# Kernel tuning notes

Hardware: AMD Instinct MI355X
Metric: run time of the kernel (lower is better)

## Reference

```python
import jax, jax.numpy as jnp
import numpy as np

B, S, E = 2, 2048, 1024
H = 16
HD = E // H           # 64
KD = 64               # k_dim
VD = 64               # v_dim
SCALE = 1.0 / np.float32(np.sqrt(KD))


def setup_inputs() -> dict:
    key = jax.random.key(0)
    ks = jax.random.split(key, 10)
    return {
        "x": jax.random.normal(ks[0], (B, S, E), dtype=jnp.float32),
        "mask": jax.random.uniform(ks[1], (S, S), dtype=jnp.float32),
        "Wq": jax.random.normal(ks[2], (HD, KD), dtype=jnp.float32) * 0.05,
        "bq": jax.random.normal(ks[3], (KD,), dtype=jnp.float32) * 0.05,
        "Wk": jax.random.normal(ks[4], (HD, KD), dtype=jnp.float32) * 0.05,
        "bk": jax.random.normal(ks[5], (KD,), dtype=jnp.float32) * 0.05,
        "Wv": jax.random.normal(ks[6], (HD, VD), dtype=jnp.float32) * 0.05,
        "bv": jax.random.normal(ks[7], (VD,), dtype=jnp.float32) * 0.05,
        "Wo": jax.random.normal(ks[8], (H * VD, E), dtype=jnp.float32) * 0.05,
        "bo": jax.random.normal(ks[9], (E,), dtype=jnp.float32) * 0.05,
    }


def reference(x, mask, Wq, bq, Wk, bk, Wv, bv, Wo, bo):
    b, s, e = x.shape
    # (B, S, E) -> (B, H, S, head_dim)
    xh = x.reshape(b, s, H, HD).transpose(0, 2, 1, 3)
    q = jnp.einsum('bhsd,dk->bhsk', xh, Wq) + bq   # (B,H,S,KD)
    k = jnp.einsum('bhsd,dk->bhsk', xh, Wk) + bk   # (B,H,S,KD)
    v = jnp.einsum('bhsd,dv->bhsv', xh, Wv) + bv   # (B,H,S,VD)
    sim = jnp.einsum('bhqk,bhsk->bhqs', q, k) * SCALE  # (B,H,S,S)
    sim = sim * mask[None, None, :, :]                  # multiplicative mask
    attn = jax.nn.softmax(sim, axis=-1)
    out = jnp.einsum('bhqs,bhsv->bhqv', attn, v)        # (B,H,S,VD)
    out = out.transpose(0, 2, 1, 3).reshape(b, s, H * VD)
    return out @ Wo + bo
```

## Files before the change

kernel.cpp:

```cpp
#include <hip/hip_runtime.h>
#include <hip/hip_bf16.h>

#define SS 2048
#define EE 1024
#define SCALE 0.125f
#define LOG2E 1.44269504088896f

typedef __attribute__((ext_vector_type(8))) short short8;
typedef __attribute__((ext_vector_type(4))) float float4v;
typedef __attribute__((ext_vector_type(4))) unsigned int uint4v;

__device__ __forceinline__ unsigned short f2bf(float f) {
  unsigned int u = __float_as_uint(f);
  unsigned int lsb = (u >> 16) & 1u;
  u += 0x7fffu + lsb;
  return (unsigned short)(u >> 16);
}
__device__ __forceinline__ unsigned int pk2bf(float a, float b) {
  __hip_bfloat162 h = __float22bfloat162_rn(float2{a, b});
  return *reinterpret_cast<unsigned int*>(&h);
}

__global__ __launch_bounds__(256) void prep_kernel(
    const float* __restrict__ mask,
    const float* __restrict__ Wq, const float* __restrict__ Wk,
    const float* __restrict__ Wv,
    unsigned short* __restrict__ maskP, unsigned short* __restrict__ W3T)
{
  __shared__ unsigned short t[64 * 65];
  int blk = blockIdx.x;
  int tid = threadIdx.x;
  if (blk < 2048) {
    int idx = blk * 256 + tid;
    int lane = idx & 63, step = (idx >> 6) & 63, qt = idx >> 12;
    int li = lane & 15, g = lane >> 4;
    const float c = SCALE * LOG2E;
    const float* mrow = mask + (size_t)(qt * 16 + li) * SS + step * 32 + g * 4;
    float4 a = *(const float4*)mrow;
    float4 bb = *(const float4*)(mrow + 16);
    uint4v o;
    o.x = pk2bf(a.x * c, a.y * c);
    o.y = pk2bf(a.z * c, a.w * c);
    o.z = pk2bf(bb.x * c, bb.y * c);
    o.w = pk2bf(bb.z * c, bb.w * c);
    *(uint4v*)(maskP + (size_t)idx * 8) = o;
    return;
  }
  int m = blk - 2048;
  const float* W = (m == 0) ? Wq : (m == 1 ? Wk : Wv);
#pragma unroll
  for (int i = 0; i < 16; ++i) {
    int e = tid + i * 256; int d = e >> 6, n = e & 63;
    t[n * 65 + d] = f2bf(W[e]);
  }
  __syncthreads();
  unsigned short* dst = W3T + m * 4096;
#pragma unroll
  for (int i = 0; i < 16; ++i) {
    int e = tid + i * 256; int n = e >> 6, d = e & 63;
    dst[n * 64 + d] = t[n * 65 + d];
  }
}

__global__ __launch_bounds__(256) void qkv_kernel(
    const float* __restrict__ x, const unsigned short* __restrict__ W3T,
    const float* __restrict__ bq, const float* __restrict__ bk,
    const float* __restrict__ bv,
    unsigned short* __restrict__ Q, unsigned short* __restrict__ Kp,
    unsigned short* __restrict__ Vf)
{
  __shared__ __align__(16) unsigned short w3t[192 * 72];
  __shared__ __align__(16) unsigned short xt[64 * 72];
  __shared__ __align__(16) unsigned short ob[12288];
  __shared__ float sBias[192];
  int tid = threadIdx.x;
  int bh = blockIdx.x >> 4;
  int s0blk = (blockIdx.x & 15) * 128;
  int b = bh >> 4, h = bh & 15;
  int wv = tid >> 6, lane = tid & 63;
  int li = lane & 15, g = lane >> 4;

#pragma unroll
  for (int i = 0; i < 6; ++i) {
    int slot = tid + i * 256;
    int row = slot >> 3, c = slot & 7;
    *(short8*)(w3t + row * 72 + c * 8) = *(const short8*)(W3T + slot * 8);
  }
  if (tid < 192) sBias[tid] = (tid < 64) ? bq[tid] : (tid < 128 ? bk[tid - 64] : bv[tid - 128]);

  for (int half = 0; half < 2; ++half) {
    int s0 = s0blk + half * 64;
    if (half) __syncthreads();
    const float* xbase = x + ((size_t)(b * SS + s0)) * EE + h * 64;
#pragma unroll
    for (int it = 0; it < 4; ++it) {
      int flat = tid + it * 256;
      int row = flat >> 4, ch = flat & 15;
      float4 v = *(const float4*)(xbase + (size_t)row * EE + ch * 4);
      uint2 u; u.x = pk2bf(v.x, v.y); u.y = pk2bf(v.z, v.w);
      *(uint2*)(xt + row * 72 + ch * 4) = u;
    }
    __syncthreads();

    int mrow = wv * 16;
    short8 af[2];
#pragma unroll
    for (int ks = 0; ks < 2; ++ks)
      af[ks] = *(const short8*)(xt + (mrow + li) * 72 + ks * 32 + g * 8);

    float4v acc[12];
#pragma unroll
    for (int i = 0; i < 12; ++i) acc[i] = (float4v){0, 0, 0, 0};
#pragma unroll
    for (int ks = 0; ks < 2; ++ks)
#pragma unroll
      for (int nb = 0; nb < 12; ++nb) {
        short8 bfr = *(const short8*)(w3t + (nb * 16 + li) * 72 + ks * 32 + g * 8);
        acc[nb] = __builtin_amdgcn_mfma_f32_16x16x32_bf16(af[ks], bfr, acc[nb], 0, 0, 0);
      }

#pragma unroll
    for (int nb = 0; nb < 12; ++nb) {
      float bias = sBias[nb * 16 + li];
      int mtx = nb >> 2, sub = nb & 3;
#pragma unroll
      for (int r = 0; r < 4; ++r) {
        unsigned short v = f2bf(acc[nb][r] + bias);
        int sl = mrow + g * 4 + r;
        int stp = sl >> 5, s5 = sl & 31;
        if (mtx == 0) {
          ob[sl * 64 + sub * 16 + li] = v;
        } else if (mtx == 1) {
          int sb = s5 >> 4, lik = s5 & 15;
          int part = sub >> 1;
          int gk = ((sub & 1) << 1) | (li >> 3);
          ob[4096 + stp * 2048 + (sb * 2 + part) * 512 + (gk * 16 + lik) * 8 + (li & 7)] = v;
        } else {
          int pos = ((s5 >> 2) & 3) * 8 + ((s5 >> 4) & 1) * 4 + (s5 & 3);
          ob[8192 + stp * 2048 + sub * 512 + ((pos >> 3) * 16 + li) * 8 + (pos & 7)] = v;
        }
      }
    }
    __syncthreads();

    unsigned short* Qg = Q + ((size_t)bh * SS + s0) * 64;
    unsigned short* Kg = Kp + (size_t)bh * 131072 + (s0 >> 5) * 2048;
    unsigned short* Vg = Vf + (size_t)bh * 131072 + (s0 >> 5) * 2048;
#pragma unroll
    for (int i = 0; i < 6; ++i) {
      int slot = tid + i * 256;
      int rgn = slot >> 9, off = (slot & 511) * 8;
      short8 v = *(const short8*)(ob + rgn * 4096 + off);
      unsigned short* dst = (rgn == 0) ? (Qg + off) : (rgn == 1 ? (Kg + off) : (Vg + off));
      *(short8*)dst = v;
    }
  }
}

__global__ __launch_bounds__(256) void attn_kernel(
    const unsigned short* __restrict__ Q, const unsigned short* __restrict__ Kp,
    const unsigned short* __restrict__ Vf, const unsigned short* __restrict__ maskP,
    unsigned short* __restrict__ AO)
{
  __shared__ __align__(16) unsigned short tr_all[4 * 32 * 72];
  int tid = threadIdx.x, wv = tid >> 6, lane = tid & 63;
  int li = lane & 15, g = lane >> 4;
  int wave_id = blockIdx.x * 4 + wv;
  int bh = wave_id >> 6;
  int q0 = (wave_id & 63) * 32;

  short8 qf[2][2];
#pragma unroll
  for (int t = 0; t < 2; ++t) {
    const unsigned short* Qb = Q + ((size_t)bh * SS + q0 + t * 16 + li) * 64;
    qf[t][0] = *(const short8*)(Qb + g * 8);
    qf[t][1] = *(const short8*)(Qb + 32 + g * 8);
  }

  const unsigned short* Kg = Kp + (size_t)bh * 131072 + lane * 8;
  const unsigned short* Vg = Vf + (size_t)bh * 131072 + lane * 8;
  const unsigned short* Mg0 = maskP + (size_t)(q0 >> 4) * 32768 + lane * 8;
  const unsigned short* Mg1 = Mg0 + 32768;

  unsigned short ov = (li == 0) ? (unsigned short)0x3F80 : (unsigned short)0;
  short8 vones = {(short)ov, (short)ov, (short)ov, (short)ov,
                  (short)ov, (short)ov, (short)ov, (short)ov};

  float4v acc[2][4];
#pragma unroll
  for (int t = 0; t < 2; ++t)
#pragma unroll
    for (int nb = 0; nb < 4; ++nb) acc[t][nb] = (float4v){0, 0, 0, 0};
  float4v accd[2] = {{0, 0, 0, 0}, {0, 0, 0, 0}};

  float4v st[2][2];

  short8 kA[4], kB[4], vA[4], vB[4];
  uint4v mA0, mA1, mB0, mB1;
  {
    short8 k0[4];
#pragma unroll
    for (int i = 0; i < 4; ++i) {
      k0[i] = *(const short8*)(Kg + i * 512);
      kA[i] = *(const short8*)(Kg + 2048 + i * 512);
      kB[i] = *(const short8*)(Kg + 2 * 2048 + i * 512);
      vA[i] = *(const short8*)(Vg + i * 512);
      vB[i] = *(const short8*)(Vg + 2048 + i * 512);
    }
    mA0 = *(const uint4v*)Mg0;
    mA1 = *(const uint4v*)Mg1;
    mB0 = *(const uint4v*)(Mg0 + 512);
    mB1 = *(const uint4v*)(Mg1 + 512);
#pragma unroll
    for (int t = 0; t < 2; ++t)
#pragma unroll
      for (int sb = 0; sb < 2; ++sb) {
        float4v s = {0, 0, 0, 0};
        s = __builtin_amdgcn_mfma_f32_16x16x32_bf16(k0[sb * 2], qf[t][0], s, 0, 0, 0);
        s = __builtin_amdgcn_mfma_f32_16x16x32_bf16(k0[sb * 2 + 1], qf[t][1], s, 0, 0, 0);
        st[t][sb] = s;
      }
  }

  auto half_step = [&](short8 (&kf)[4], short8 (&vf)[4], uint4v& m0c, uint4v& m1c,
                       int kn, int vn, int mn) {
    short8 pf[2];
#pragma unroll
    for (int t = 0; t < 2; ++t) {
      uint4v pw2;
#pragma unroll
      for (int sb = 0; sb < 2; ++sb) {
#pragma unroll
        for (int hh = 0; hh < 2; ++hh) {
          unsigned int mm = (t == 0) ? m0c[sb * 2 + hh] : m1c[sb * 2 + hh];
          float p0 = __builtin_amdgcn_exp2f(st[t][sb][2 * hh] * __uint_as_float(mm << 16));
          float p1 = __builtin_amdgcn_exp2f(st[t][sb][2 * hh + 1] * __uint_as_float(mm & 0xffff0000u));
          pw2[sb * 2 + hh] = pk2bf(p0, p1);
        }
      }
      pf[t] = *(short8*)&pw2;
    }
    m0c = *(const uint4v*)(Mg0 + (size_t)mn * 512);
    m1c = *(const uint4v*)(Mg1 + (size_t)mn * 512);
#pragma unroll
    for (int t = 0; t < 2; ++t)
#pragma unroll
      for (int sb = 0; sb < 2; ++sb) {
        float4v s = {0, 0, 0, 0};
        s = __builtin_amdgcn_mfma_f32_16x16x32_bf16(kf[sb * 2], qf[t][0], s, 0, 0, 0);
        s = __builtin_amdgcn_mfma_f32_16x16x32_bf16(kf[sb * 2 + 1], qf[t][1], s, 0, 0, 0);
        st[t][sb] = s;
      }
#pragma unroll
    for (int i = 0; i < 4; ++i)
      kf[i] = *(const short8*)(Kg + (size_t)kn * 2048 + i * 512);
#pragma unroll
    for (int nb = 0; nb < 4; ++nb) {
      acc[0][nb] = __builtin_amdgcn_mfma_f32_16x16x32_bf16(vf[nb], pf[0], acc[0][nb], 0, 0, 0);
      acc[1][nb] = __builtin_amdgcn_mfma_f32_16x16x32_bf16(vf[nb], pf[1], acc[1][nb], 0, 0, 0);
    }
    accd[0] = __builtin_amdgcn_mfma_f32_16x16x32_bf16(vones, pf[0], accd[0], 0, 0, 0);
    accd[1] = __builtin_amdgcn_mfma_f32_16x16x32_bf16(vones, pf[1], accd[1], 0, 0, 0);
#pragma unroll
    for (int i = 0; i < 4; ++i)
      vf[i] = *(const short8*)(Vg + (size_t)vn * 2048 + i * 512);
  };

  for (int su = 0; su < 32; ++su) {
    half_step(kA, vA, mA0, mA1, (2 * su + 3) & 63, (2 * su + 2) & 63, (2 * su + 2) & 63);
    half_step(kB, vB, mB0, mB1, (2 * su + 4) & 63, (2 * su + 3) & 63, (2 * su + 3) & 63);
  }

  unsigned short* tr = tr_all + wv * (32 * 72);
#pragma unroll
  for (int t = 0; t < 2; ++t) {
    float den = __shfl(accd[t][0], li, 64);
    float rd = 1.0f / den;
#pragma unroll
    for (int nb = 0; nb < 4; ++nb) {
      int base = (t * 16 + li) * 72 + nb * 16 + g * 4;
      *(unsigned int*)(tr + base)     = pk2bf(acc[t][nb][0] * rd, acc[t][nb][1] * rd);
      *(unsigned int*)(tr + base + 2) = pk2bf(acc[t][nb][2] * rd, acc[t][nb][3] * rd);
    }
  }
  asm volatile("s_waitcnt lgkmcnt(0)" ::: "memory");

  int b = bh >> 4, h = bh & 15;
  int rrow = lane >> 3, part = lane & 7;
#pragma unroll
  for (int i = 0; i < 4; ++i) {
    int row = i * 8 + rrow;
    short8 o = *(const short8*)(tr + row * 72 + part * 8);
    *(short8*)(AO + ((size_t)(b * SS + q0 + row)) * EE + h * 64 + part * 8) = o;
  }
}

__global__ __launch_bounds__(256) void out_gemm(
    const unsigned short* __restrict__ AO, const float* __restrict__ Wo,
    const float* __restrict__ bo, float* __restrict__ out)
{
  __shared__ __align__(16) unsigned short at[128 * 72];
  __shared__ __align__(16) unsigned short bt[64 * 72];
  int tid = threadIdx.x, wv = tid >> 6, lane = tid & 63;
  int li = lane & 15, g = lane >> 4;
  int m0 = (blockIdx.x >> 4) * 128;
  int n0 = (blockIdx.x & 15) * 64;
  int wm = (wv & 1) * 64, wn = (wv >> 1) * 32;

  const unsigned short* Ag = AO + (size_t)m0 * 1024;
  const float* Bg = Wo + n0;
  int srow = tid >> 3, scol = (tid & 7) * 8;
  int bkrow = tid >> 4, bch = tid & 15;

  short8 apre[4];
  float4 bpre[4];
  auto ldst = [&](int k0) {
#pragma unroll
    for (int i = 0; i < 4; ++i)
      apre[i] = *(const short8*)(Ag + (size_t)(srow + i * 32) * 1024 + k0 + scol);
#pragma unroll
    for (int i = 0; i < 4; ++i)
      bpre[i] = *(const float4*)(Bg + (size_t)(k0 + bkrow + i * 16) * 1024 + bch * 4);
  };

  float4v acc[4][2];
#pragma unroll
  for (int mt = 0; mt < 4; ++mt)
#pragma unroll
    for (int nt = 0; nt < 2; ++nt) acc[mt][nt] = (float4v){0, 0, 0, 0};

  ldst(0);
  for (int k0 = 0; k0 < 1024; k0 += 64) {
    __syncthreads();
#pragma unroll
    for (int i = 0; i < 4; ++i)
      *(short8*)(at + (srow + i * 32) * 72 + scol) = apre[i];
#pragma unroll
    for (int i = 0; i < 4; ++i) {
      int kr = bkrow + i * 16;
      float4 v = bpre[i];
      bt[(bch * 4 + 0) * 72 + kr] = f2bf(v.x);
      bt[(bch * 4 + 1) * 72 + kr] = f2bf(v.y);
      bt[(bch * 4 + 2) * 72 + kr] = f2bf(v.z);
      bt[(bch * 4 + 3) * 72 + kr] = f2bf(v.w);
    }
    int nk = (k0 + 64 < 1024) ? k0 + 64 : 0;
    ldst(nk);
    __syncthreads();
#pragma unroll
    for (int ks = 0; ks < 2; ++ks) {
      short8 afr[4], bfr[2];
#pragma unroll
      for (int mt = 0; mt < 4; ++mt)
        afr[mt] = *(const short8*)(at + (wm + mt * 16 + li) * 72 + ks * 32 + g * 8);
#pragma unroll
      for (int nt = 0; nt < 2; ++nt)
        bfr[nt] = *(const short8*)(bt + (wn + nt * 16 + li) * 72 + ks * 32 + g * 8);
#pragma unroll
      for (int mt = 0; mt < 4; ++mt)
#pragma unroll
        for (int nt = 0; nt < 2; ++nt)
          acc[mt][nt] = __builtin_amdgcn_mfma_f32_16x16x32_bf16(afr[mt], bfr[nt], acc[mt][nt], 0, 0, 0);
    }
  }
#pragma unroll
  for (int nt = 0; nt < 2; ++nt) {
    float bof = bo[n0 + wn + nt * 16 + li];
#pragma unroll
    for (int mt = 0; mt < 4; ++mt)
#pragma unroll
      for (int r = 0; r < 4; ++r)
        out[(size_t)(m0 + wm + mt * 16 + g * 4 + r) * 1024 + n0 + wn + nt * 16 + li] =
            acc[mt][nt][r] + bof;
  }
}

extern "C" void kernel_launch(void* const* d_in, const int* in_sizes, int n_in,
                              void* d_out, int out_size, void* d_ws, size_t ws_size,
                              hipStream_t stream) {
  const float* x    = (const float*)d_in[0];
  const float* mask = (const float*)d_in[1];
  const float* Wq   = (const float*)d_in[2];
  const float* bq   = (const float*)d_in[3];
  const float* Wk   = (const float*)d_in[4];
  const float* bk   = (const float*)d_in[5];
  const float* Wv   = (const float*)d_in[6];
  const float* bv   = (const float*)d_in[7];
  const float* Wo   = (const float*)d_in[8];
  const float* bo   = (const float*)d_in[9];
  float* out = (float*)d_out;

  unsigned short* ws = (unsigned short*)d_ws;
  unsigned short* Q     = ws;
  unsigned short* Kp    = ws + 4194304;
  unsigned short* Vf    = ws + 8388608;
  unsigned short* AO    = ws + 12582912;
  unsigned short* maskP = ws + 16777216;
  unsigned short* W3T = AO;

  prep_kernel<<<2051, 256, 0, stream>>>(mask, Wq, Wk, Wv, maskP, W3T);
  qkv_kernel<<<512, 256, 0, stream>>>(x, W3T, bq, bk, bv, Q, Kp, Vf);
  attn_kernel<<<512, 256, 0, stream>>>(Q, Kp, Vf, maskP, AO);
  out_gemm<<<512, 256, 0, stream>>>(AO, Wo, bo, out);
}
```

Before: 191.5 us.

## Stage K/V tiles in shared memory cooperatively and remap blocks for L2 locality

Instead of each wave loading its own K and V tiles straight from global memory into registers, the four waves of a block now cooperatively load one K/V tile pair into a double-buffered LDS region and all read from it. This cuts redundant global traffic by four, since all waves in a block share the same head. Blocks are also remapped so consecutively scheduled blocks spread across heads, to change L2/XCD locality. The cost is a __syncthreads per step and LDS read latency in the inner loop, plus the register-level prefetch depth is reduced.

```diff
diff --git a/kernel.cpp b/kernel.cpp
--- a/kernel.cpp
+++ b/kernel.cpp
@@ -162,10 +162,11 @@
     const unsigned short* __restrict__ Vf, const unsigned short* __restrict__ maskP,
     unsigned short* __restrict__ AO)
 {
-  __shared__ __align__(16) unsigned short tr_all[4 * 32 * 72];
+  __shared__ __align__(16) unsigned short smem[9216];
   int tid = threadIdx.x, wv = tid >> 6, lane = tid & 63;
   int li = lane & 15, g = lane >> 4;
-  int wave_id = blockIdx.x * 4 + wv;
+  int virt = (blockIdx.x & 7) * 64 + (blockIdx.x >> 3);
+  int wave_id = virt * 4 + wv;
   int bh = wave_id >> 6;
   int q0 = (wave_id & 63) * 32;
 
@@ -177,8 +178,12 @@
     qf[t][1] = *(const short8*)(Qb + 32 + g * 8);
   }
 
-  const unsigned short* Kg = Kp + (size_t)bh * 131072 + lane * 8;
-  const unsigned short* Vg = Vf + (size_t)bh * 131072 + lane * 8;
+  const unsigned short* stgsrc =
+      ((wv < 2) ? (Kp + (size_t)bh * 131072) : (Vf + (size_t)bh * 131072)) +
+      (wv & 1) * 1024 + lane * 8;
+  unsigned short* srd = smem + lane * 8;
+  unsigned short* swr = smem + wv * 1024 + lane * 8;
+
   const unsigned short* Mg0 = maskP + (size_t)(q0 >> 4) * 32768 + lane * 8;
   const unsigned short* Mg1 = Mg0 + 32768;
 
@@ -194,23 +199,26 @@
   float4v accd[2] = {{0, 0, 0, 0}, {0, 0, 0, 0}};
 
   float4v st[2][2];
-
-  short8 kA[4], kB[4], vA[4], vB[4];
-  uint4v mA0, mA1, mB0, mB1;
+  short8 vf[4];
+  uint4v mc0, mc1;
+
+  mc0 = *(const uint4v*)Mg0;
+  mc1 = *(const uint4v*)Mg1;
+  {
+    short8 a0 = *(const short8*)(stgsrc);
+    short8 a1 = *(const short8*)(stgsrc + 512);
+    short8 b0 = *(const short8*)(stgsrc + 2048);
+    short8 b1 = *(const short8*)(stgsrc + 2048 + 512);
+    *(short8*)(swr + 0) = a0;
+    *(short8*)(swr + 512) = a1;
+    *(short8*)(swr + 4096) = b0;
+    *(short8*)(swr + 4096 + 512) = b1;
+  }
+  __syncthreads();
   {
     short8 k0[4];
 #pragma unroll
-    for (int i = 0; i < 4; ++i) {
-      k0[i] = *(const short8*)(Kg + i * 512);
-      kA[i] = *(const short8*)(Kg + 2048 + i * 512);
-      kB[i] = *(const short8*)(Kg + 2 * 2048 + i * 512);
-      vA[i] = *(const short8*)(Vg + i * 512);
-      vB[i] = *(const short8*)(Vg + 2048 + i * 512);
-    }
-    mA0 = *(const uint4v*)Mg0;
-    mA1 = *(const uint4v*)Mg1;
-    mB0 = *(const uint4v*)(Mg0 + 512);
-    mB1 = *(const uint4v*)(Mg1 + 512);
+    for (int i = 0; i < 4; ++i) k0[i] = *(const short8*)(srd + i * 512);
 #pragma unroll
     for (int t = 0; t < 2; ++t)
 #pragma unroll
@@ -220,40 +228,39 @@
         s = __builtin_amdgcn_mfma_f32_16x16x32_bf16(k0[sb * 2 + 1], qf[t][1], s, 0, 0, 0);
         st[t][sb] = s;
       }
-  }
-
-  auto half_step = [&](short8 (&kf)[4], short8 (&vf)[4], uint4v& m0c, uint4v& m1c,
-                       int kn, int vn, int mn) {
+#pragma unroll
+    for (int i = 0; i < 4; ++i) vf[i] = *(const short8*)(srd + 2048 + i * 512);
+  }
+  __syncthreads();
+
+  auto body = [&](int s, int pcur, bool do_stage) {
+    short8 sg0, sg1;
+    if (do_stage) {
+      const unsigned short* gs = stgsrc + (size_t)(s + 2) * 2048;
+      sg0 = *(const short8*)gs;
+      sg1 = *(const short8*)(gs + 512);
+    }
+    short8 kf[4];
+#pragma unroll
+    for (int i = 0; i < 4; ++i)
+      kf[i] = *(const short8*)(srd + pcur * 4096 + i * 512);
     short8 pf[2];
 #pragma unroll
     for (int t = 0; t < 2; ++t) {
       uint4v pw2;
 #pragma unroll
-      for (int sb = 0; sb < 2; ++sb) {
+      for (int sb = 0; sb < 2; ++sb)
 #pragma unroll
         for (int hh = 0; hh < 2; ++hh) {
-          unsigned int mm = (t == 0) ? m0c[sb * 2 + hh] : m1c[sb * 2 + hh];
+          unsigned int mm = (t == 0) ? mc0[sb * 2 + hh] : mc1[sb * 2 + hh];
           float p0 = __builtin_amdgcn_exp2f(st[t][sb][2 * hh] * __uint_as_float(mm << 16));
           float p1 = __builtin_amdgcn_exp2f(st[t][sb][2 * hh + 1] * __uint_as_float(mm & 0xffff0000u));
           pw2[sb * 2 + hh] = pk2bf(p0, p1);
         }
-      }
       pf[t] = *(short8*)&pw2;
     }
-    m0c = *(const uint4v*)(Mg0 + (size_t)mn * 512);
-    m1c = *(const uint4v*)(Mg1 + (size_t)mn * 512);
-#pragma unroll
-    for (int t = 0; t < 2; ++t)
-#pragma unroll
-      for (int sb = 0; sb < 2; ++sb) {
-        float4v s = {0, 0, 0, 0};
-        s = __builtin_amdgcn_mfma_f32_16x16x32_bf16(kf[sb * 2], qf[t][0], s, 0, 0, 0);
-        s = __builtin_amdgcn_mfma_f32_16x16x32_bf16(kf[sb * 2 + 1], qf[t][1], s, 0, 0, 0);
-        st[t][sb] = s;
-      }
-#pragma unroll
-    for (int i = 0; i < 4; ++i)
-      kf[i] = *(const short8*)(Kg + (size_t)kn * 2048 + i * 512);
+    mc0 = *(const uint4v*)(Mg0 + (size_t)(s + 1) * 512);
+    mc1 = *(const uint4v*)(Mg1 + (size_t)(s + 1) * 512);
 #pragma unroll
     for (int nb = 0; nb < 4; ++nb) {
       acc[0][nb] = __builtin_amdgcn_mfma_f32_16x16x32_bf16(vf[nb], pf[0], acc[0][nb], 0, 0, 0);
@@ -263,15 +270,56 @@
     accd[1] = __builtin_amdgcn_mfma_f32_16x16x32_bf16(vones, pf[1], accd[1], 0, 0, 0);
 #pragma unroll
     for (int i = 0; i < 4; ++i)
-      vf[i] = *(const short8*)(Vg + (size_t)vn * 2048 + i * 512);
+      vf[i] = *(const short8*)(srd + pcur * 4096 + 2048 + i * 512);
+#pragma unroll
+    for (int t = 0; t < 2; ++t)
+#pragma unroll
+      for (int sb = 0; sb < 2; ++sb) {
+        float4v s2 = {0, 0, 0, 0};
+        s2 = __builtin_amdgcn_mfma_f32_16x16x32_bf16(kf[sb * 2], qf[t][0], s2, 0, 0, 0);
+        s2 = __builtin_amdgcn_mfma_f32_16x16x32_bf16(kf[sb * 2 + 1], qf[t][1], s2, 0, 0, 0);
+        st[t][sb] = s2;
+      }
+    if (do_stage) {
+      *(short8*)(swr + (pcur ^ 1) * 4096) = sg0;
+      *(short8*)(swr + (pcur ^ 1) * 4096 + 512) = sg1;
+    }
+    __syncthreads();
   };
 
-  for (int su = 0; su < 32; ++su) {
-    half_step(kA, vA, mA0, mA1, (2 * su + 3) & 63, (2 * su + 2) & 63, (2 * su + 2) & 63);
-    half_step(kB, vB, mB0, mB1, (2 * su + 4) & 63, (2 * su + 3) & 63, (2 * su + 3) & 63);
-  }
-
-  unsigned short* tr = tr_all + wv * (32 * 72);
+#pragma unroll 1
+  for (int su = 0; su < 31; ++su) {
+    body(2 * su, 1, true);
+    body(2 * su + 1, 0, true);
+  }
+  body(62, 1, false);
+  {
+    short8 pf[2];
+#pragma unroll
+    for (int t = 0; t < 2; ++t) {
+      uint4v pw2;
+#pragma unroll
+      for (int sb = 0; sb < 2; ++sb)
+#pragma unroll
+        for (int hh = 0; hh < 2; ++hh) {
+          unsigned int mm = (t == 0) ? mc0[sb * 2 + hh] : mc1[sb * 2 + hh];
+          float p0 = __builtin_amdgcn_exp2f(st[t][sb][2 * hh] * __uint_as_float(mm << 16));
+          float p1 = __builtin_amdgcn_exp2f(st[t][sb][2 * hh + 1] * __uint_as_float(mm & 0xffff0000u));
+          pw2[sb * 2 + hh] = pk2bf(p0, p1);
+        }
+      pf[t] = *(short8*)&pw2;
+    }
+#pragma unroll
+    for (int nb = 0; nb < 4; ++nb) {
+      acc[0][nb] = __builtin_amdgcn_mfma_f32_16x16x32_bf16(vf[nb], pf[0], acc[0][nb], 0, 0, 0);
+      acc[1][nb] = __builtin_amdgcn_mfma_f32_16x16x32_bf16(vf[nb], pf[1], acc[1][nb], 0, 0, 0);
+    }
+    accd[0] = __builtin_amdgcn_mfma_f32_16x16x32_bf16(vones, pf[0], accd[0], 0, 0, 0);
+    accd[1] = __builtin_amdgcn_mfma_f32_16x16x32_bf16(vones, pf[1], accd[1], 0, 0, 0);
+  }
+  __syncthreads();
+
+  unsigned short* tr = smem + wv * (32 * 72);
 #pragma unroll
   for (int t = 0; t < 2; ++t) {
     float den = __shfl(accd[t][0], li, 64);
```

New measurement: 192.4 us. Within noise of the previous version (+0.4%).

## Pre-transpose Wo to bf16 in prep kernel and widen out_gemm tile

Applied to the files above, without the earlier changes.

The prep kernel gains 256 blocks that convert Wo to bf16 and write it transposed (N-major), so out_gemm can load B tiles with vector short8 loads instead of converting fp32 and doing scalar transposed LDS stores on every k-step of every block. out_gemm also grows its N tile from 64 to 128 (4x4 MFMA accumulators per wave), halving the grid to 256 blocks and cutting the number of times AO is re-read. This costs extra workspace, a larger prep launch, more registers per thread and fewer blocks to fill the GPU.

```diff
diff --git a/kernel.cpp b/kernel.cpp
--- a/kernel.cpp
+++ b/kernel.cpp
@@ -24,8 +24,9 @@
 __global__ __launch_bounds__(256) void prep_kernel(
     const float* __restrict__ mask,
     const float* __restrict__ Wq, const float* __restrict__ Wk,
-    const float* __restrict__ Wv,
-    unsigned short* __restrict__ maskP, unsigned short* __restrict__ W3T)
+    const float* __restrict__ Wv, const float* __restrict__ Wo,
+    unsigned short* __restrict__ maskP, unsigned short* __restrict__ W3T,
+    unsigned short* __restrict__ WoT)
 {
   __shared__ unsigned short t[64 * 65];
   int blk = blockIdx.x;
@@ -46,19 +47,35 @@
     *(uint4v*)(maskP + (size_t)idx * 8) = o;
     return;
   }
-  int m = blk - 2048;
-  const float* W = (m == 0) ? Wq : (m == 1 ? Wk : Wv);
+  if (blk < 2051) {
+    int m = blk - 2048;
+    const float* W = (m == 0) ? Wq : (m == 1 ? Wk : Wv);
+#pragma unroll
+    for (int i = 0; i < 16; ++i) {
+      int e = tid + i * 256; int d = e >> 6, n = e & 63;
+      t[n * 65 + d] = f2bf(W[e]);
+    }
+    __syncthreads();
+    unsigned short* dst = W3T + m * 4096;
+#pragma unroll
+    for (int i = 0; i < 16; ++i) {
+      int e = tid + i * 256; int n = e >> 6, d = e & 63;
+      dst[n * 64 + d] = t[n * 65 + d];
+    }
+    return;
+  }
+  int wblk = blk - 2051;
+  int k0 = (wblk >> 4) * 64, n0 = (wblk & 15) * 64;
 #pragma unroll
   for (int i = 0; i < 16; ++i) {
-    int e = tid + i * 256; int d = e >> 6, n = e & 63;
-    t[n * 65 + d] = f2bf(W[e]);
+    int e = tid + i * 256; int kk = e >> 6, nn = e & 63;
+    t[nn * 65 + kk] = f2bf(Wo[(size_t)(k0 + kk) * 1024 + n0 + nn]);
   }
   __syncthreads();
-  unsigned short* dst = W3T + m * 4096;
 #pragma unroll
   for (int i = 0; i < 16; ++i) {
-    int e = tid + i * 256; int n = e >> 6, d = e & 63;
-    dst[n * 64 + d] = t[n * 65 + d];
+    int e = tid + i * 256; int nn = e >> 6, kk = e & 63;
+    WoT[(size_t)(n0 + nn) * 1024 + k0 + kk] = t[nn * 65 + kk];
   }
 }
 
@@ -296,75 +313,65 @@
 }
 
 __global__ __launch_bounds__(256) void out_gemm(
-    const unsigned short* __restrict__ AO, const float* __restrict__ Wo,
+    const unsigned short* __restrict__ AO, const unsigned short* __restrict__ WoT,
     const float* __restrict__ bo, float* __restrict__ out)
 {
   __shared__ __align__(16) unsigned short at[128 * 72];
-  __shared__ __align__(16) unsigned short bt[64 * 72];
+  __shared__ __align__(16) unsigned short bt[128 * 72];
   int tid = threadIdx.x, wv = tid >> 6, lane = tid & 63;
   int li = lane & 15, g = lane >> 4;
-  int m0 = (blockIdx.x >> 4) * 128;
-  int n0 = (blockIdx.x & 15) * 64;
-  int wm = (wv & 1) * 64, wn = (wv >> 1) * 32;
+  int n0 = (blockIdx.x & 7) * 128;
+  int m0 = (blockIdx.x >> 3) * 128;
+  int wm = (wv & 1) * 64, wn = (wv >> 1) * 64;
 
   const unsigned short* Ag = AO + (size_t)m0 * 1024;
-  const float* Bg = Wo + n0;
+  const unsigned short* Bg = WoT + (size_t)n0 * 1024;
   int srow = tid >> 3, scol = (tid & 7) * 8;
-  int bkrow = tid >> 4, bch = tid & 15;
-
-  short8 apre[4];
-  float4 bpre[4];
+
+  short8 apre[4], bpre[4];
   auto ldst = [&](int k0) {
 #pragma unroll
-    for (int i = 0; i < 4; ++i)
+    for (int i = 0; i < 4; ++i) {
       apre[i] = *(const short8*)(Ag + (size_t)(srow + i * 32) * 1024 + k0 + scol);
-#pragma unroll
-    for (int i = 0; i < 4; ++i)
-      bpre[i] = *(const float4*)(Bg + (size_t)(k0 + bkrow + i * 16) * 1024 + bch * 4);
+      bpre[i] = *(const short8*)(Bg + (size_t)(srow + i * 32) * 1024 + k0 + scol);
+    }
   };
 
-  float4v acc[4][2];
+  float4v acc[4][4];
 #pragma unroll
   for (int mt = 0; mt < 4; ++mt)
 #pragma unroll
-    for (int nt = 0; nt < 2; ++nt) acc[mt][nt] = (float4v){0, 0, 0, 0};
+    for (int nt = 0; nt < 4; ++nt) acc[mt][nt] = (float4v){0, 0, 0, 0};
 
   ldst(0);
   for (int k0 = 0; k0 < 1024; k0 += 64) {
     __syncthreads();
 #pragma unroll
-    for (int i = 0; i < 4; ++i)
+    for (int i = 0; i < 4; ++i) {
       *(short8*)(at + (srow + i * 32) * 72 + scol) = apre[i];
-#pragma unroll
-    for (int i = 0; i < 4; ++i) {
-      int kr = bkrow + i * 16;
-      float4 v = bpre[i];
-      bt[(bch * 4 + 0) * 72 + kr] = f2bf(v.x);
-      bt[(bch * 4 + 1) * 72 + kr] = f2bf(v.y);
-      bt[(bch * 4 + 2) * 72 + kr] = f2bf(v.z);
-      bt[(bch * 4 + 3) * 72 + kr] = f2bf(v.w);
+      *(short8*)(bt + (srow + i * 32) * 72 + scol) = bpre[i];
     }
     int nk = (k0 + 64 < 1024) ? k0 + 64 : 0;
     ldst(nk);
     __syncthreads();
 #pragma unroll
     for (int ks = 0; ks < 2; ++ks) {
-      short8 afr[4], bfr[2];
+      short8 afr[4], bfr[4];
 #pragma unroll
       for (int mt = 0; mt < 4; ++mt)
         afr[mt] = *(const short8*)(at + (wm + mt * 16 + li) * 72 + ks * 32 + g * 8);
 #pragma unroll
-      for (int nt = 0; nt < 2; ++nt)
+      for (int nt = 0; nt < 4; ++nt)
         bfr[nt] = *(const short8*)(bt + (wn + nt * 16 + li) * 72 + ks * 32 + g * 8);
 #pragma unroll
       for (int mt = 0; mt < 4; ++mt)
 #pragma unroll
-        for (int nt = 0; nt < 2; ++nt)
+        for (int nt = 0; nt < 4; ++nt)
           acc[mt][nt] = __builtin_amdgcn_mfma_f32_16x16x32_bf16(afr[mt], bfr[nt], acc[mt][nt], 0, 0, 0);
     }
   }
 #pragma unroll
-  for (int nt = 0; nt < 2; ++nt) {
+  for (int nt = 0; nt < 4; ++nt) {
     float bof = bo[n0 + wn + nt * 16 + li];
 #pragma unroll
     for (int mt = 0; mt < 4; ++mt)
@@ -396,10 +403,11 @@
   unsigned short* Vf    = ws + 8388608;
   unsigned short* AO    = ws + 12582912;
   unsigned short* maskP = ws + 16777216;
+  unsigned short* WoT   = ws + 20971520;
   unsigned short* W3T = AO;
 
-  prep_kernel<<<2051, 256, 0, stream>>>(mask, Wq, Wk, Wv, maskP, W3T);
+  prep_kernel<<<2307, 256, 0, stream>>>(mask, Wq, Wk, Wv, Wo, maskP, W3T, WoT);
   qkv_kernel<<<512, 256, 0, stream>>>(x, W3T, bq, bk, bv, Q, Kp, Vf);
   attn_kernel<<<512, 256, 0, stream>>>(Q, Kp, Vf, maskP, AO);
-  out_gemm<<<512, 256, 0, stream>>>(AO, Wo, bo, out);
-}
+  out_gemm<<<256, 256, 0, stream>>>(AO, WoT, bo, out);
+}
```

Result: faster. 172.3 us (-10.0%).

## Merge prep and QKV kernels; pre-transpose Wo to bf16 for out GEMM

Applied to the files above, without the earlier changes.

Folds the mask preprocessing and QKV projection into one launch, with each QKV block converting the small Wq/Wk/Wv weights itself, which removes one kernel launch and the W3T round trip. Extra blocks in the same launch convert Wo to a transposed bf16 copy in workspace. The output GEMM then loads bf16 rows with vector loads instead of fp32 loads with per-element conversion and scattered LDS stores. The cost is an added pass over Wo each call, redundant weight conversion in every QKV block, and a larger shared-memory footprint for the fused kernel, which may lower occupancy.

```diff
diff --git a/kernel.cpp b/kernel.cpp
--- a/kernel.cpp
+++ b/kernel.cpp
@@ -21,70 +21,75 @@
   return *reinterpret_cast<unsigned int*>(&h);
 }
 
-__global__ __launch_bounds__(256) void prep_kernel(
-    const float* __restrict__ mask,
+__global__ __launch_bounds__(256) void fused_qkv(
+    const float* __restrict__ x,
     const float* __restrict__ Wq, const float* __restrict__ Wk,
     const float* __restrict__ Wv,
-    unsigned short* __restrict__ maskP, unsigned short* __restrict__ W3T)
-{
-  __shared__ unsigned short t[64 * 65];
-  int blk = blockIdx.x;
-  int tid = threadIdx.x;
-  if (blk < 2048) {
-    int idx = blk * 256 + tid;
-    int lane = idx & 63, step = (idx >> 6) & 63, qt = idx >> 12;
-    int li = lane & 15, g = lane >> 4;
-    const float c = SCALE * LOG2E;
-    const float* mrow = mask + (size_t)(qt * 16 + li) * SS + step * 32 + g * 4;
-    float4 a = *(const float4*)mrow;
-    float4 bb = *(const float4*)(mrow + 16);
-    uint4v o;
-    o.x = pk2bf(a.x * c, a.y * c);
-    o.y = pk2bf(a.z * c, a.w * c);
-    o.z = pk2bf(bb.x * c, bb.y * c);
-    o.w = pk2bf(bb.z * c, bb.w * c);
-    *(uint4v*)(maskP + (size_t)idx * 8) = o;
-    return;
-  }
-  int m = blk - 2048;
-  const float* W = (m == 0) ? Wq : (m == 1 ? Wk : Wv);
-#pragma unroll
-  for (int i = 0; i < 16; ++i) {
-    int e = tid + i * 256; int d = e >> 6, n = e & 63;
-    t[n * 65 + d] = f2bf(W[e]);
-  }
-  __syncthreads();
-  unsigned short* dst = W3T + m * 4096;
-#pragma unroll
-  for (int i = 0; i < 16; ++i) {
-    int e = tid + i * 256; int n = e >> 6, d = e & 63;
-    dst[n * 64 + d] = t[n * 65 + d];
-  }
-}
-
-__global__ __launch_bounds__(256) void qkv_kernel(
-    const float* __restrict__ x, const unsigned short* __restrict__ W3T,
     const float* __restrict__ bq, const float* __restrict__ bk,
     const float* __restrict__ bv,
+    const float* __restrict__ mask, const float* __restrict__ Wo,
     unsigned short* __restrict__ Q, unsigned short* __restrict__ Kp,
-    unsigned short* __restrict__ Vf)
+    unsigned short* __restrict__ Vf,
+    unsigned short* __restrict__ maskP, unsigned short* __restrict__ WoT)
 {
   __shared__ __align__(16) unsigned short w3t[192 * 72];
   __shared__ __align__(16) unsigned short xt[64 * 72];
   __shared__ __align__(16) unsigned short ob[12288];
   __shared__ float sBias[192];
+  __shared__ unsigned short t[64 * 65];
+  int blk = blockIdx.x;
   int tid = threadIdx.x;
-  int bh = blockIdx.x >> 4;
-  int s0blk = (blockIdx.x & 15) * 128;
+
+  if (blk >= 512) {
+    if (blk < 2560) {
+      int idx = (blk - 512) * 256 + tid;
+      int lane = idx & 63, step = (idx >> 6) & 63, qt = idx >> 12;
+      int li = lane & 15, g = lane >> 4;
+      const float c = SCALE * LOG2E;
+      const float* mrow = mask + (size_t)(qt * 16 + li) * SS + step * 32 + g * 4;
+      float4 a = *(const float4*)mrow;
+      float4 bb = *(const float4*)(mrow + 16);
+      uint4v o;
+      o.x = pk2bf(a.x * c, a.y * c);
+      o.y = pk2bf(a.z * c, a.w * c);
+      o.z = pk2bf(bb.x * c, bb.y * c);
+      o.w = pk2bf(bb.z * c, bb.w * c);
+      *(uint4v*)(maskP + (size_t)idx * 8) = o;
+      return;
+    }
+    int wblk = blk - 2560;
+    int k0 = (wblk >> 4) * 64, n0 = (wblk & 15) * 64;
+#pragma unroll
+    for (int i = 0; i < 16; ++i) {
+      int e = tid + i * 256; int kk = e >> 6, nn = e & 63;
+      t[nn * 65 + kk] = f2bf(Wo[(size_t)(k0 + kk) * 1024 + n0 + nn]);
+    }
+    __syncthreads();
+#pragma unroll
+    for (int i = 0; i < 16; ++i) {
+      int e = tid + i * 256; int nn = e >> 6, kk = e & 63;
+      WoT[(size_t)(n0 + nn) * 1024 + k0 + kk] = t[nn * 65 + kk];
+    }
+    return;
+  }
+
+  int bh = blk >> 4;
+  int s0blk = (blk & 15) * 128;
   int b = bh >> 4, h = bh & 15;
   int wv = tid >> 6, lane = tid & 63;
   int li = lane & 15, g = lane >> 4;
 
-#pragma unroll
-  for (int i = 0; i < 6; ++i) {
-    int slot = tid + i * 256;
-    int row = slot >> 3, c = slot & 7;
-    *(short8*)(w3t + row * 72 + c * 8) = *(const short8*)(W3T + slot * 8);
+  {
+    const float* Ws[3] = {Wq, Wk, Wv};
+#pragma unroll
+    for (int m = 0; m < 3; ++m) {
+      const float* W = Ws[m];
+#pragma unroll
+      for (int i = 0; i < 16; ++i) {
+        int e = tid + i * 256; int d = e >> 6, n = e & 63;
+        w3t[(m * 64 + n) * 72 + d] = f2bf(W[e]);
+      }
+    }
   }
   if (tid < 192) sBias[tid] = (tid < 64) ? bq[tid] : (tid < 128 ? bk[tid - 64] : bv[tid - 128]);
 
@@ -296,7 +301,7 @@
 }
 
 __global__ __launch_bounds__(256) void out_gemm(
-    const unsigned short* __restrict__ AO, const float* __restrict__ Wo,
+    const unsigned short* __restrict__ AO, const unsigned short* __restrict__ WoT,
     const float* __restrict__ bo, float* __restrict__ out)
 {
   __shared__ __align__(16) unsigned short at[128 * 72];
@@ -308,19 +313,20 @@
   int wm = (wv & 1) * 64, wn = (wv >> 1) * 32;
 
   const unsigned short* Ag = AO + (size_t)m0 * 1024;
-  const float* Bg = Wo + n0;
+  const unsigned short* Bg = WoT + (size_t)n0 * 1024;
   int srow = tid >> 3, scol = (tid & 7) * 8;
-  int bkrow = tid >> 4, bch = tid & 15;
-
-  short8 apre[4];
-  float4 bpre[4];
+
+  short8 apre[4], bpre[2];
   auto ldst = [&](int k0) {
 #pragma unroll
     for (int i = 0; i < 4; ++i)
       apre[i] = *(const short8*)(Ag + (size_t)(srow + i * 32) * 1024 + k0 + scol);
 #pragma unroll
-    for (int i = 0; i < 4; ++i)
-      bpre[i] = *(const float4*)(Bg + (size_t)(k0 + bkrow + i * 16) * 1024 + bch * 4);
+    for (int i = 0; i < 2; ++i) {
+      int slot = tid + i * 256;
+      int row = slot >> 3, col = (slot & 7) * 8;
+      bpre[i] = *(const short8*)(Bg + (size_t)row * 1024 + k0 + col);
+    }
   };
 
   float4v acc[4][2];
@@ -336,13 +342,10 @@
     for (int i = 0; i < 4; ++i)
       *(short8*)(at + (srow + i * 32) * 72 + scol) = apre[i];
 #pragma unroll
-    for (int i = 0; i < 4; ++i) {
-      int kr = bkrow + i * 16;
-      float4 v = bpre[i];
-      bt[(bch * 4 + 0) * 72 + kr] = f2bf(v.x);
-      bt[(bch * 4 + 1) * 72 + kr] = f2bf(v.y);
-      bt[(bch * 4 + 2) * 72 + kr] = f2bf(v.z);
-      bt[(bch * 4 + 3) * 72 + kr] = f2bf(v.w);
+    for (int i = 0; i < 2; ++i) {
+      int slot = tid + i * 256;
+      int row = slot >> 3, col = (slot & 7) * 8;
+      *(short8*)(bt + row * 72 + col) = bpre[i];
     }
     int nk = (k0 + 64 < 1024) ? k0 + 64 : 0;
     ldst(nk);
@@ -396,10 +399,10 @@
   unsigned short* Vf    = ws + 8388608;
   unsigned short* AO    = ws + 12582912;
   unsigned short* maskP = ws + 16777216;
-  unsigned short* W3T = AO;
-
-  prep_kernel<<<2051, 256, 0, stream>>>(mask, Wq, Wk, Wv, maskP, W3T);
-  qkv_kernel<<<512, 256, 0, stream>>>(x, W3T, bq, bk, bv, Q, Kp, Vf);
+  unsigned short* WoT   = ws + 20971520;
+
+  fused_qkv<<<2816, 256, 0, stream>>>(x, Wq, Wk, Wv, bq, bk, bv, mask, Wo,
+                                      Q, Kp, Vf, maskP, WoT);
   attn_kernel<<<512, 256, 0, stream>>>(Q, Kp, Vf, maskP, AO);
-  out_gemm<<<512, 256, 0, stream>>>(AO, Wo, bo, out);
-}
+  out_gemm<<<512, 256, 0, stream>>>(AO, WoT, bo, out);
+}
```

Result: faster. 173.3 us (-9.5%).
